# Kernel tuning notes

Measured on AMD Instinct MI355X. Metric: run time of the kernel, lower is better.

The kernel has to match this reference:

```python
import jax, jax.numpy as jnp
import numpy as np

N = 3072          # n_vertices
D = 512           # embedding_size (hardcoded in module)
ALPHA = 0.2       # LeakyReLU slope
AVG_DEG = 32
NEG_INF = -9e15
N_ITERS = 10
TRIPLET_MARGIN = 400.0


def setup_inputs() -> dict:
    key = jax.random.key(0)
    ks = jax.random.split(key, 14)
    s = 0.05  # weight init scale
    emb = jax.random.normal(ks[0], (N, D), dtype=jnp.float32) * 0.1
    # symmetric 0/1 adjacency, no self loops, density ~ AVG_DEG/N
    u = jax.random.uniform(ks[1], (N, N))
    A = jnp.triu((u < (AVG_DEG / N)).astype(jnp.float32), 1)
    adj = A + A.T
    rn = lambda k, shp: jax.random.normal(k, shp, dtype=jnp.float32) * s
    return {
        "embeddings": emb,
        "adj": adj,
        "W_n": rn(ks[2], (D, D)), "a_src_n": rn(ks[3], (D,)), "a_dst_n": rn(ks[4], (D,)),
        "W_nn": rn(ks[5], (D, D)), "a_src_nn": rn(ks[6], (D,)), "a_dst_nn": rn(ks[7], (D,)),
        "W_u": rn(ks[8], (2 * D, D)), "b_u": jnp.zeros((D,), dtype=jnp.float32),
        "W_g": rn(ks[9], (D, D)), "a_src_g": rn(ks[10], (D,)), "a_dst_g": rn(ks[11], (D,)),
    }


def _gat_attention(h, adj, W, a_src, a_dst):
    # standard pyGAT layer: Wh = hW; e_ij = LeakyReLU(a_src.Wh_i + a_dst.Wh_j)
    Wh = h @ W                                   # [N, D]
    e = jax.nn.leaky_relu((Wh @ a_src)[:, None] + (Wh @ a_dst)[None, :], ALPHA)
    att = jax.nn.softmax(jnp.where(adj > 0, e, NEG_INF), axis=1)  # [N, N]
    return att, Wh


def reference(embeddings, adj, W_n, a_src_n, a_dst_n, W_nn, a_src_nn, a_dst_nn,
              W_u, b_u, W_g, a_src_g, a_dst_g):
    n = embeddings.shape[0]
    inv_adj = 1.0 - adj - jnp.eye(n, dtype=adj.dtype)  # non-neighbors, no self
    emb = embeddings
    for _ in range(N_ITERS):
        att_n, Wh_n = _gat_attention(emb, adj, W_n, a_src_n, a_dst_n)
        neigh = jax.nn.elu(att_n @ Wh_n)               # concat=True -> ELU
        att_nn, Wh_nn = _gat_attention(emb, inv_adj, W_nn, a_src_nn, a_dst_nn)
        non_neigh = jax.nn.elu(att_nn @ Wh_nn)
        cat = jnp.concatenate([neigh, non_neigh], axis=1)  # [N, 2D]
        emb = jax.nn.relu(emb + cat @ W_u + b_u)
    sq = jnp.sum(emb * emb, axis=1)
    d2 = sq[:, None] + sq[None, :] - 2.0 * (emb @ emb.T)
    dist = jnp.sqrt(jnp.maximum(d2, 1e-12))            # [N, N]
    embedding_loss = jnp.sum(dist * (-adj))
    triplet_loss = jnp.maximum(embedding_loss + TRIPLET_MARGIN, 0.0)
    # glimpse layer returns the attention matrix itself
    att_g, _ = _gat_attention(emb, adj, W_g, a_src_g, a_dst_g)
    confidence = jnp.max(att_g, axis=1)
    log_conf = jnp.mean(jnp.log(confidence + 1e-8) - jnp.log(1e-8))
    return jnp.stack([triplet_loss, embedding_loss, log_conf])
```

## Files before the change

kernel.cpp:

```cpp
#include <hip/hip_runtime.h>
#include <math.h>

#define N_V 3072
#define D_E 512
#define EDGE_CAP 128
constexpr float LRELU_ALPHA = 0.2f;
constexpr float NEG_INF_F = -9e15f;

typedef __attribute__((ext_vector_type(8))) short bf16x8;
typedef __attribute__((ext_vector_type(4))) float f32x4;
typedef __attribute__((ext_vector_type(4))) unsigned short ushort4v;
typedef __attribute__((ext_vector_type(2))) unsigned short ushort2v;

__device__ inline unsigned short f2bf(float f) {
    union { float f; unsigned int u; } x; x.f = f;
    unsigned int r = x.u + 0x7fffu + ((x.u >> 16) & 1u);
    return (unsigned short)(r >> 16);
}
__device__ inline float bf2f(unsigned short b) {
    union { unsigned int u; float f; } x; x.u = ((unsigned int)b) << 16;
    return x.f;
}

__device__ inline void xcd_swizzle(int& bx, int& by) {
    int gx = gridDim.x, nwg = gx * gridDim.y;
    int flat = by * gx + bx;
    int q = nwg >> 3;
    int swz = (flat & 7) * q + (flat >> 3);
    bx = swz % gx; by = swz / gx;
}

template<int EPI>
__global__ __launch_bounds__(256) void gemm_bf16(
    const unsigned short* __restrict__ A,
    const unsigned short* __restrict__ BT,
    int M, int N, int K,
    unsigned short* __restrict__ C0, int ldc0,
    unsigned short* __restrict__ C1,
    const float* __restrict__ addv,
    const float* __restrict__ bias,
    float* __restrict__ Cf)
{
    constexpr int BM = 128, BN = 64, BK = 64;
    __shared__ unsigned short As[BM * BK];
    __shared__ unsigned short Bs[BN * BK];
    const int tid  = threadIdx.x;
    int bxi = blockIdx.x, byi = blockIdx.y;
    xcd_swizzle(bxi, byi);
    const int bm   = byi * BM, bn = bxi * BN;
    const int lane = tid & 63, wid = tid >> 6;
    const int wr   = wid >> 1, wc = wid & 1;
    const int lr   = lane & 15, lk = lane >> 4;

    f32x4 acc[4][2];
    #pragma unroll
    for (int i = 0; i < 4; ++i)
        #pragma unroll
        for (int j = 0; j < 2; ++j)
            acc[i][j] = (f32x4)(0.f);

    auto asp = (__attribute__((address_space(3))) unsigned short*)As;
    auto bsp = (__attribute__((address_space(3))) unsigned short*)Bs;

    for (int k0 = 0; k0 < K; k0 += BK) {
        #pragma unroll
        for (int l = 0; l < 4; ++l) {
            int li = l * 256 + tid;
            int row = li >> 3, slot = li & 7;
            int gs = slot ^ (row & 7);
            __builtin_amdgcn_global_load_lds(
                (const __attribute__((address_space(1))) void*)(A + (size_t)(bm + row) * K + k0 + gs * 8),
                (__attribute__((address_space(3))) void*)(asp + li * 8), 16, 0, 0);
        }
        #pragma unroll
        for (int l = 0; l < 2; ++l) {
            int li = l * 256 + tid;
            int row = li >> 3, slot = li & 7;
            int gs = slot ^ (row & 7);
            __builtin_amdgcn_global_load_lds(
                (const __attribute__((address_space(1))) void*)(BT + (size_t)(bn + row) * K + k0 + gs * 8),
                (__attribute__((address_space(3))) void*)(bsp + li * 8), 16, 0, 0);
        }
        __syncthreads();

        #pragma unroll
        for (int ks = 0; ks < 2; ++ks) {
            bf16x8 af[4], bfr[2];
            #pragma unroll
            for (int fm = 0; fm < 4; ++fm) {
                int row = wr * 64 + fm * 16 + lr;
                int sl = (ks * 4 + lk) ^ (row & 7);
                af[fm] = *(const bf16x8*)(As + row * BK + sl * 8);
            }
            #pragma unroll
            for (int fn = 0; fn < 2; ++fn) {
                int col = wc * 32 + fn * 16 + lr;
                int sl = (ks * 4 + lk) ^ (col & 7);
                bfr[fn] = *(const bf16x8*)(Bs + col * BK + sl * 8);
            }
            #pragma unroll
            for (int fm = 0; fm < 4; ++fm)
                #pragma unroll
                for (int fn = 0; fn < 2; ++fn)
                    acc[fm][fn] = __builtin_amdgcn_mfma_f32_16x16x32_bf16(
                        af[fm], bfr[fn], acc[fm][fn], 0, 0, 0);
        }
        __syncthreads();
    }

    #pragma unroll
    for (int fm = 0; fm < 4; ++fm) {
        #pragma unroll
        for (int fn = 0; fn < 2; ++fn) {
            int row0 = bm + wr * 64 + fm * 16 + lk * 4;
            int col  = bn + wc * 32 + fn * 16 + lr;
            f32x4 v = acc[fm][fn];
            if (EPI == 2) {
                #pragma unroll
                for (int r = 0; r < 4; ++r) {
                    float x = v[r] + addv[(size_t)(row0 + r) * N + col] + bias[col];
                    x = x > 0.f ? x : 0.f;
                    Cf[(size_t)(row0 + r) * N + col] = x;
                    C0[(size_t)(row0 + r) * ldc0 + col] = f2bf(x);
                }
            } else {
                if (col < 512) {
                    #pragma unroll
                    for (int r = 0; r < 4; ++r)
                        C0[(size_t)(row0 + r) * ldc0 + col] = f2bf(v[r]);
                } else {
                    ushort4v p;
                    p.x = f2bf(v[0]); p.y = f2bf(v[1]);
                    p.z = f2bf(v[2]); p.w = f2bf(v[3]);
                    *(ushort4v*)(C1 + (size_t)(col - 512) * M + row0) = p;
                }
            }
        }
    }
}

__global__ __launch_bounds__(256) void gemm_bf16_sk(
    const unsigned short* __restrict__ A,
    const unsigned short* __restrict__ BT,
    int M, int N, int K,
    float* __restrict__ Cp)
{
    constexpr int BM = 128, BN = 64, BK = 64;
    __shared__ unsigned short As[BM * BK];
    __shared__ unsigned short Bs[BN * BK];
    const int tid  = threadIdx.x;
    int bxi = blockIdx.x, byi = blockIdx.y;
    xcd_swizzle(bxi, byi);
    const int bm   = byi * BM, bn = bxi * BN;
    const int kz   = blockIdx.z;
    const int kh   = K >> 1;
    const int kbeg = kz * kh, kend = kbeg + kh;
    const int lane = tid & 63, wid = tid >> 6;
    const int wr   = wid >> 1, wc = wid & 1;
    const int lr   = lane & 15, lk = lane >> 4;

    f32x4 acc[4][2];
    #pragma unroll
    for (int i = 0; i < 4; ++i)
        #pragma unroll
        for (int j = 0; j < 2; ++j)
            acc[i][j] = (f32x4)(0.f);

    auto asp = (__attribute__((address_space(3))) unsigned short*)As;
    auto bsp = (__attribute__((address_space(3))) unsigned short*)Bs;

    for (int k0 = kbeg; k0 < kend; k0 += BK) {
        #pragma unroll
        for (int l = 0; l < 4; ++l) {
            int li = l * 256 + tid;
            int row = li >> 3, slot = li & 7;
            int gs = slot ^ (row & 7);
            __builtin_amdgcn_global_load_lds(
                (const __attribute__((address_space(1))) void*)(A + (size_t)(bm + row) * K + k0 + gs * 8),
                (__attribute__((address_space(3))) void*)(asp + li * 8), 16, 0, 0);
        }
        #pragma unroll
        for (int l = 0; l < 2; ++l) {
            int li = l * 256 + tid;
            int row = li >> 3, slot = li & 7;
            int gs = slot ^ (row & 7);
            __builtin_amdgcn_global_load_lds(
                (const __attribute__((address_space(1))) void*)(BT + (size_t)(bn + row) * K + k0 + gs * 8),
                (__attribute__((address_space(3))) void*)(bsp + li * 8), 16, 0, 0);
        }
        __syncthreads();

        #pragma unroll
        for (int ks = 0; ks < 2; ++ks) {
            bf16x8 af[4], bfr[2];
            #pragma unroll
            for (int fm = 0; fm < 4; ++fm) {
                int row = wr * 64 + fm * 16 + lr;
                int sl = (ks * 4 + lk) ^ (row & 7);
                af[fm] = *(const bf16x8*)(As + row * BK + sl * 8);
            }
            #pragma unroll
            for (int fn = 0; fn < 2; ++fn) {
                int col = wc * 32 + fn * 16 + lr;
                int sl = (ks * 4 + lk) ^ (col & 7);
                bfr[fn] = *(const bf16x8*)(Bs + col * BK + sl * 8);
            }
            #pragma unroll
            for (int fm = 0; fm < 4; ++fm)
                #pragma unroll
                for (int fn = 0; fn < 2; ++fn)
                    acc[fm][fn] = __builtin_amdgcn_mfma_f32_16x16x32_bf16(
                        af[fm], bfr[fn], acc[fm][fn], 0, 0, 0);
        }
        __syncthreads();
    }

    float* Cz = Cp + (size_t)kz * M * N;
    #pragma unroll
    for (int fm = 0; fm < 4; ++fm) {
        #pragma unroll
        for (int fn = 0; fn < 2; ++fn) {
            int row0 = bm + wr * 64 + fm * 16 + lk * 4;
            int col  = bn + wc * 32 + fn * 16 + lr;
            #pragma unroll
            for (int r = 0; r < 4; ++r)
                Cz[(size_t)(row0 + r) * N + col] = acc[fm][fn][r];
        }
    }
}

__global__ __launch_bounds__(256) void elu_combine(
    const float* __restrict__ p0, const float* __restrict__ p1,
    unsigned short* __restrict__ cat)
{
    int idx = blockIdx.x * 256 + threadIdx.x;
    float4 a = ((const float4*)p0)[idx];
    float4 b = ((const float4*)p1)[idx];
    int r = idx >> 7;
    int c = (idx & 127) * 4;
    float v[4] = { a.x + b.x, a.y + b.y, a.z + b.z, a.w + b.w };
    ushort4v o;
    #pragma unroll
    for (int q = 0; q < 4; ++q) {
        float x = v[q];
        x = x > 0.f ? x : (expf(x) - 1.f);
        ((unsigned short*)&o)[q] = f2bf(x);
    }
    *(ushort4v*)(cat + (size_t)r * (2 * D_E) + D_E + c) = o;
}

__global__ __launch_bounds__(256) void convT_f32_bf16(
    const float* __restrict__ W, unsigned short* __restrict__ WT, int K, int Nw)
{
    int k = blockIdx.x * 256 + threadIdx.x;
    int n = blockIdx.y;
    if (k < K) WT[(size_t)n * K + k] = f2bf(W[(size_t)k * Nw + n]);
}

__global__ __launch_bounds__(256) void conv_bf16(
    const float* __restrict__ X, unsigned short* __restrict__ Y, int n)
{
    int i = blockIdx.x * 256 + threadIdx.x;
    if (i < n) Y[i] = f2bf(X[i]);
}

__global__ __launch_bounds__(256) void build_graph(
    const float* __restrict__ adj, int* __restrict__ edges,
    int* __restrict__ deg, unsigned int* __restrict__ bitmask)
{
    const int i = blockIdx.x, t = threadIdx.x;
    __shared__ int cnts[256];
    unsigned int word = 0;
    int c = 0;
    if (t < 96) {
        #pragma unroll
        for (int b = 0; b < 32; ++b) {
            int j = t * 32 + b;
            if (adj[(size_t)i * N_V + j] > 0.f) { word |= (1u << b); ++c; }
        }
    }
    cnts[t] = c;
    __syncthreads();
    for (int o = 1; o < 256; o <<= 1) {
        int add = (t >= o) ? cnts[t - o] : 0;
        __syncthreads();
        cnts[t] += add;
        __syncthreads();
    }
    int base = cnts[t] - c;
    if (t < 96) {
        int k = 0;
        #pragma unroll
        for (int b = 0; b < 32; ++b) {
            if ((word >> b) & 1u) {
                int pos = base + k;
                if (pos < EDGE_CAP) edges[(size_t)i * EDGE_CAP + pos] = t * 32 + b;
                ++k;
            }
        }
        bitmask[(size_t)i * 96 + t] = word;
    }
    if (t == 0) deg[i] = cnts[255] < EDGE_CAP ? cnts[255] : EDGE_CAP;
}

__global__ __launch_bounds__(256) void matvec6(
    const float* __restrict__ W_n, const float* __restrict__ W_nn,
    const float* __restrict__ W_g,
    const float* __restrict__ as_n, const float* __restrict__ ad_n,
    const float* __restrict__ as_nn, const float* __restrict__ ad_nn,
    const float* __restrict__ as_g, const float* __restrict__ ad_g,
    float* __restrict__ wv)
{
    const int wave = threadIdx.x >> 6, lane = threadIdx.x & 63;
    const int r = blockIdx.x * 4 + wave;
    float a0 = 0, a1 = 0, a2 = 0, a3 = 0, a4 = 0, a5 = 0;
    #pragma unroll
    for (int k = 0; k < 8; ++k) {
        int c = lane + k * 64;
        float wn = W_n[(size_t)r * D_E + c];
        float wm = W_nn[(size_t)r * D_E + c];
        float wg = W_g[(size_t)r * D_E + c];
        a0 = fmaf(wn, as_n[c], a0);  a1 = fmaf(wn, ad_n[c], a1);
        a2 = fmaf(wm, as_nn[c], a2); a3 = fmaf(wm, ad_nn[c], a3);
        a4 = fmaf(wg, as_g[c], a4);  a5 = fmaf(wg, ad_g[c], a5);
    }
    #pragma unroll
    for (int off = 32; off; off >>= 1) {
        a0 += __shfl_down(a0, off); a1 += __shfl_down(a1, off);
        a2 += __shfl_down(a2, off); a3 += __shfl_down(a3, off);
        a4 += __shfl_down(a4, off); a5 += __shfl_down(a5, off);
    }
    if (lane == 0) {
        wv[0 * D_E + r] = a0; wv[1 * D_E + r] = a1;
        wv[2 * D_E + r] = a2; wv[3 * D_E + r] = a3;
        wv[4 * D_E + r] = a4; wv[5 * D_E + r] = a5;
    }
}

template<int NV>
__global__ __launch_bounds__(256) void sd_dots(
    const unsigned short* __restrict__ emb, const float* __restrict__ wv,
    float* __restrict__ outs)
{
    const int wave = threadIdx.x >> 6, lane = threadIdx.x & 63;
    const int i = blockIdx.x * 4 + wave;
    float acc[NV];
    #pragma unroll
    for (int v = 0; v < NV; ++v) acc[v] = 0.f;
    #pragma unroll
    for (int k = 0; k < 8; ++k) {
        int c = lane + k * 64;
        float x = bf2f(emb[(size_t)i * D_E + c]);
        #pragma unroll
        for (int v = 0; v < NV; ++v) acc[v] = fmaf(x, wv[v * D_E + c], acc[v]);
    }
    #pragma unroll
    for (int off = 32; off; off >>= 1)
        #pragma unroll
        for (int v = 0; v < NV; ++v) acc[v] += __shfl_down(acc[v], off);
    if (lane == 0)
        #pragma unroll
        for (int v = 0; v < NV; ++v) outs[v * N_V + i] = acc[v];
}

__global__ __launch_bounds__(256) void nn_sm_gather(
    const unsigned int* __restrict__ bitmask,
    const int* __restrict__ edges, const int* __restrict__ deg,
    const float* __restrict__ sd,
    const unsigned short* __restrict__ Whn,
    unsigned short* __restrict__ att, unsigned short* __restrict__ cat)
{
    const int t = threadIdx.x;
    __shared__ float red[256];
    if (blockIdx.x < N_V) {
        const int i = blockIdx.x;
        const float* s = sd + 2 * N_V;
        const float* dvec = sd + 3 * N_V;
        __shared__ unsigned int mrow[96];
        if (t < 96) mrow[t] = bitmask[(size_t)i * 96 + t];
        __syncthreads();
        const float si = s[i];
        const float4* dv4 = (const float4*)dvec;
        float e[3][4];
        float mloc = -3.4e38f;
        #pragma unroll
        for (int l = 0; l < 3; ++l) {
            int jv = t + l * 256;
            float4 d = dv4[jv];
            int j0 = jv * 4;
            unsigned int w = mrow[j0 >> 5];
            #pragma unroll
            for (int c = 0; c < 4; ++c) {
                int j = j0 + c;
                bool keep = (((w >> (j & 31)) & 1u) == 0u) && (j != i);
                float x = si + ((const float*)&d)[c];
                x = x > 0.f ? x : LRELU_ALPHA * x;
                e[l][c] = keep ? x : NEG_INF_F;
                mloc = fmaxf(mloc, e[l][c]);
            }
        }
        red[t] = mloc; __syncthreads();
        for (int o = 128; o; o >>= 1) {
            if (t < o) red[t] = fmaxf(red[t], red[t + o]);
            __syncthreads();
        }
        float m = red[0]; __syncthreads();
        float zloc = 0.f;
        #pragma unroll
        for (int l = 0; l < 3; ++l)
            #pragma unroll
            for (int c = 0; c < 4; ++c) { e[l][c] = expf(e[l][c] - m); zloc += e[l][c]; }
        red[t] = zloc; __syncthreads();
        for (int o = 128; o; o >>= 1) {
            if (t < o) red[t] += red[t + o];
            __syncthreads();
        }
        const float zinv = 1.f / red[0];
        #pragma unroll
        for (int l = 0; l < 3; ++l) {
            int jv = t + l * 256;
            ushort4v p;
            p.x = f2bf(e[l][0] * zinv); p.y = f2bf(e[l][1] * zinv);
            p.z = f2bf(e[l][2] * zinv); p.w = f2bf(e[l][3] * zinv);
            *(ushort4v*)(att + (size_t)i * N_V + (size_t)jv * 4) = p;
        }
    } else {
        const int i = blockIdx.x - N_V;
        const float* s = sd;
        const float* dvec = sd + N_V;
        const int cnt = deg[i];
        __shared__ float p[EDGE_CAP];
        __shared__ int lst[EDGE_CAP];
        float ev = -3.4e38f;
        if (t < cnt) {
            int j = edges[(size_t)i * EDGE_CAP + t];
            lst[t] = j;
            float x = s[i] + dvec[j];
            x = x > 0.f ? x : LRELU_ALPHA * x;
            p[t] = x;
            ev = x;
        }
        red[t] = ev; __syncthreads();
        for (int o = 128; o; o >>= 1) {
            if (t < o) red[t] = fmaxf(red[t], red[t + o]);
            __syncthreads();
        }
        float m = red[0]; __syncthreads();
        float pe = 0.f;
        if (t < cnt) { pe = expf(p[t] - m); p[t] = pe; }
        red[t] = pe; __syncthreads();
        for (int o = 128; o; o >>= 1) {
            if (t < o) red[t] += red[t + o];
            __syncthreads();
        }
        const float zinv = 1.f / red[0];
        float a0 = 0.f, a1 = 0.f;
        for (int e = 0; e < cnt; ++e) {
            int j = lst[e];
            float w = p[e] * zinv;
            ushort2v h = *(const ushort2v*)(Whn + (size_t)j * D_E + t * 2);
            a0 = fmaf(w, bf2f(h.x), a0);
            a1 = fmaf(w, bf2f(h.y), a1);
        }
        a0 = a0 > 0.f ? a0 : (expf(a0) - 1.f);
        a1 = a1 > 0.f ? a1 : (expf(a1) - 1.f);
        ushort2v o2; o2.x = f2bf(a0); o2.y = f2bf(a1);
        *(ushort2v*)(cat + (size_t)i * (2 * D_E) + t * 2) = o2;
    }
}

__global__ __launch_bounds__(256) void rowsumsq(
    const float* __restrict__ emb, float* __restrict__ sq)
{
    const int wave = threadIdx.x >> 6, lane = threadIdx.x & 63;
    const int row = blockIdx.x * 4 + wave;
    const float* w = emb + (size_t)row * D_E;
    float ss = 0.f;
    #pragma unroll
    for (int k = 0; k < 8; ++k) {
        float x = w[lane + k * 64];
        ss = fmaf(x, x, ss);
    }
    #pragma unroll
    for (int off = 32; off; off >>= 1) ss += __shfl_down(ss, off);
    if (lane == 0) sq[row] = ss;
}

__global__ __launch_bounds__(256) void edge_loss2(
    const int* __restrict__ edges, const int* __restrict__ deg,
    const float* __restrict__ emb, const float* __restrict__ sq,
    float* __restrict__ accum)
{
    __shared__ float wsum[4];
    const int i = blockIdx.x, t = threadIdx.x;
    const int wave = t >> 6, lane = t & 63;
    const int cnt = deg[i];
    float ei[8];
    #pragma unroll
    for (int k = 0; k < 8; ++k) ei[k] = emb[(size_t)i * D_E + lane + k * 64];
    float sum = 0.f;
    for (int e = wave; e < cnt; e += 4) {
        int j = edges[(size_t)i * EDGE_CAP + e];
        float dot = 0.f;
        #pragma unroll
        for (int k = 0; k < 8; ++k)
            dot = fmaf(ei[k], emb[(size_t)j * D_E + lane + k * 64], dot);
        #pragma unroll
        for (int off = 32; off; off >>= 1) dot += __shfl_down(dot, off);
        if (lane == 0) {
            float d2 = sq[i] + sq[j] - 2.f * dot;
            sum += sqrtf(fmaxf(d2, 1e-12f));
        }
    }
    if (lane == 0) wsum[wave] = sum;
    __syncthreads();
    if (t == 0) atomicAdd(accum, -(wsum[0] + wsum[1] + wsum[2] + wsum[3]));
}

__global__ __launch_bounds__(256) void conf_kernel(
    const unsigned int* __restrict__ bitmask, const float* __restrict__ s,
    const float* __restrict__ dvec, float* __restrict__ accum)
{
    const int i = blockIdx.x, t = threadIdx.x;
    __shared__ unsigned int mrow[96];
    __shared__ float red[256];
    if (t < 96) mrow[t] = bitmask[(size_t)i * 96 + t];
    __syncthreads();
    const float si = s[i];
    const float4* dv4 = (const float4*)dvec;
    float e[3][4];
    float mloc = -3.4e38f;
    #pragma unroll
    for (int l = 0; l < 3; ++l) {
        int jv = t + l * 256;
        float4 d = dv4[jv];
        int j0 = jv * 4;
        unsigned int w = mrow[j0 >> 5];
        #pragma unroll
        for (int c = 0; c < 4; ++c) {
            int j = j0 + c;
            bool keep = ((w >> (j & 31)) & 1u) != 0u;
            float x = si + ((const float*)&d)[c];
            x = x > 0.f ? x : LRELU_ALPHA * x;
            e[l][c] = keep ? x : NEG_INF_F;
            mloc = fmaxf(mloc, e[l][c]);
        }
    }
    red[t] = mloc; __syncthreads();
    for (int o = 128; o; o >>= 1) {
        if (t < o) red[t] = fmaxf(red[t], red[t + o]);
        __syncthreads();
    }
    float m = red[0]; __syncthreads();
    float zloc = 0.f;
    #pragma unroll
    for (int l = 0; l < 3; ++l)
        #pragma unroll
        for (int c = 0; c < 4; ++c) zloc += expf(e[l][c] - m);
    red[t] = zloc; __syncthreads();
    for (int o = 128; o; o >>= 1) {
        if (t < o) red[t] += red[t + o];
        __syncthreads();
    }
    if (t == 0) atomicAdd(accum, logf(1.f / red[0] + 1e-8f));
}

__global__ void finalize(const float* __restrict__ accum, float* __restrict__ out)
{
    float loss = accum[0];
    out[0] = fmaxf(loss + 400.f, 0.f);
    out[1] = loss;
    out[2] = accum[1] / (float)N_V - logf(1e-8f);
}

extern "C" void kernel_launch(void* const* d_in, const int* in_sizes, int n_in,
                              void* d_out, int out_size, void* d_ws, size_t ws_size,
                              hipStream_t stream) {
    const float* emb_in   = (const float*)d_in[0];
    const float* adj      = (const float*)d_in[1];
    const float* W_n      = (const float*)d_in[2];
    const float* a_src_n  = (const float*)d_in[3];
    const float* a_dst_n  = (const float*)d_in[4];
    const float* W_nn     = (const float*)d_in[5];
    const float* a_src_nn = (const float*)d_in[6];
    const float* a_dst_nn = (const float*)d_in[7];
    const float* W_u      = (const float*)d_in[8];
    const float* b_u      = (const float*)d_in[9];
    const float* W_g      = (const float*)d_in[10];
    const float* a_src_g  = (const float*)d_in[11];
    const float* a_dst_g  = (const float*)d_in[12];
    float* out = (float*)d_out;

    char* p = (char*)d_ws;
    auto alloc = [&](size_t bytes) { char* r = p; p += (bytes + 255) & ~(size_t)255; return r; };

    unsigned short* att_nn  = (unsigned short*)alloc((size_t)N_V * N_V * 2);
    float*          Cp      = (float*)alloc((size_t)2 * N_V * D_E * 4);
    unsigned short* Whn     = (unsigned short*)alloc((size_t)N_V * D_E * 2);
    unsigned short* WhTnn   = (unsigned short*)alloc((size_t)D_E * N_V * 2);
    unsigned short* cat_bf  = (unsigned short*)alloc((size_t)N_V * 2 * D_E * 2);
    float*          embf[2] = { (float*)alloc((size_t)N_V * D_E * 4),
                                (float*)alloc((size_t)N_V * D_E * 4) };
    unsigned short* embb[2] = { (unsigned short*)alloc((size_t)N_V * D_E * 2),
                                (unsigned short*)alloc((size_t)N_V * D_E * 2) };
    unsigned short* W2T     = (unsigned short*)alloc((size_t)(2 * D_E) * D_E * 2);
    unsigned short* WuT     = (unsigned short*)alloc((size_t)D_E * (2 * D_E) * 2);
    float*          wv      = (float*)alloc(6 * D_E * 4);
    float*          sd      = (float*)alloc(4 * N_V * 4);
    float*          sdg     = (float*)alloc(2 * N_V * 4);
    float*          sq      = (float*)alloc(N_V * 4);
    int*            edges   = (int*)alloc((size_t)N_V * EDGE_CAP * 4);
    int*            deg     = (int*)alloc(N_V * 4);
    unsigned int*   bitmask = (unsigned int*)alloc((size_t)N_V * 96 * 4);
    float*          accum   = (float*)alloc(2 * 4);

    dim3 blk(256);

    convT_f32_bf16<<<dim3(2, D_E), blk, 0, stream>>>(W_n, W2T, D_E, D_E);
    convT_f32_bf16<<<dim3(2, D_E), blk, 0, stream>>>(W_nn, W2T + (size_t)D_E * D_E, D_E, D_E);
    convT_f32_bf16<<<dim3(4, D_E), blk, 0, stream>>>(W_u, WuT, 2 * D_E, D_E);
    conv_bf16<<<(N_V * D_E) / 256, blk, 0, stream>>>(emb_in, embb[0], N_V * D_E);
    hipMemcpyAsync(embf[0], emb_in, (size_t)N_V * D_E * 4, hipMemcpyDeviceToDevice, stream);
    hipMemsetAsync(accum, 0, 2 * sizeof(float), stream);
    build_graph<<<N_V, blk, 0, stream>>>(adj, edges, deg, bitmask);
    matvec6<<<D_E / 4, blk, 0, stream>>>(W_n, W_nn, W_g, a_src_n, a_dst_n,
                                         a_src_nn, a_dst_nn, a_src_g, a_dst_g, wv);

    dim3 gW2(16, N_V / 128);
    dim3 gG(8, N_V / 128);
    dim3 gSK(8, N_V / 128, 2);

    int cur = 0;
    for (int it = 0; it < 10; ++it) {
        int nxt = cur ^ 1;
        sd_dots<4><<<N_V / 4, blk, 0, stream>>>(embb[cur], wv, sd);
        gemm_bf16<4><<<gW2, blk, 0, stream>>>(embb[cur], W2T, N_V, 2 * D_E, D_E,
                                              Whn, D_E, WhTnn, nullptr, nullptr, nullptr);
        nn_sm_gather<<<2 * N_V, blk, 0, stream>>>(bitmask, edges, deg, sd,
                                                  Whn, att_nn, cat_bf);
        gemm_bf16_sk<<<gSK, blk, 0, stream>>>(att_nn, WhTnn, N_V, D_E, N_V, Cp);
        elu_combine<<<(N_V * D_E) / (4 * 256), blk, 0, stream>>>(
            Cp, Cp + (size_t)N_V * D_E, cat_bf);
        gemm_bf16<2><<<gG, blk, 0, stream>>>(cat_bf, WuT, N_V, D_E, 2 * D_E,
                                             embb[nxt], D_E, nullptr, embf[cur], b_u, embf[nxt]);
        cur = nxt;
    }

    rowsumsq<<<N_V / 4, blk, 0, stream>>>(embf[cur], sq);
    edge_loss2<<<N_V, blk, 0, stream>>>(edges, deg, embf[cur], sq, accum);
    sd_dots<2><<<N_V / 4, blk, 0, stream>>>(embb[cur], wv + 4 * D_E, sdg);
    conf_kernel<<<N_V, blk, 0, stream>>>(bitmask, sdg, sdg + N_V, accum + 1);

    finalize<<<1, 1, 0, stream>>>(accum, out);
}
```

Measured before the change: 942.9 us.

## Generate non-neighbor attention on the fly inside GEMM via factored softmax

The non-neighbor attention matrix is no longer written to a dense N×N bf16 buffer. The LeakyReLU softmax is factored into per-row scalars (R1, R0, computed from a global max and the row sums minus the neighbor corrections) and per-column exponentials (ed1, ed0). The GEMM then builds A-tiles in registers from the adjacency bitmask. This removes a large write and read of the attention matrix each iteration, and the GEMM moves to 128x128 tiles with split-K of 4. In exchange it adds top2/zrow kernels, redundant per-element exp-free recomputation in the GEMM, bitmask loads from global inside the inner loop, and possible numerical differences from the global-max factorisation. The edge loss kernel is also reworked to use 16-lane groups with shared memory.

```diff
diff --git a/kernel.cpp b/kernel.cpp
--- a/kernel.cpp
+++ b/kernel.cpp
@@ -139,48 +139,52 @@
     }
 }
 
-__global__ __launch_bounds__(256) void gemm_bf16_sk(
-    const unsigned short* __restrict__ A,
+template<int SPLITK>
+__global__ __launch_bounds__(256) void gemm_nn(
     const unsigned short* __restrict__ BT,
-    int M, int N, int K,
+    const float* __restrict__ dvec,
+    const float* __restrict__ ed1v, const float* __restrict__ ed0v,
+    const float* __restrict__ svec,
+    const float* __restrict__ R1v, const float* __restrict__ R0v,
+    const unsigned int* __restrict__ bitmask,
     float* __restrict__ Cp)
 {
-    constexpr int BM = 128, BN = 64, BK = 64;
-    __shared__ unsigned short As[BM * BK];
+    constexpr int BM = 128, BN = 128, BK = 64;
     __shared__ unsigned short Bs[BN * BK];
-    const int tid  = threadIdx.x;
+    __shared__ float dsh[BK], e1sh[BK], e0sh[BK];
+    const int tid = threadIdx.x;
     int bxi = blockIdx.x, byi = blockIdx.y;
     xcd_swizzle(bxi, byi);
-    const int bm   = byi * BM, bn = bxi * BN;
-    const int kz   = blockIdx.z;
-    const int kh   = K >> 1;
-    const int kbeg = kz * kh, kend = kbeg + kh;
+    const int bm = byi * BM, bn = bxi * BN;
+    const int K  = N_V;
+    const int kh = K / SPLITK;
+    const int kbeg = blockIdx.z * kh, kend = kbeg + kh;
     const int lane = tid & 63, wid = tid >> 6;
-    const int wr   = wid >> 1, wc = wid & 1;
-    const int lr   = lane & 15, lk = lane >> 4;
-
-    f32x4 acc[4][2];
+    const int wr = wid >> 1, wc = wid & 1;
+    const int lr = lane & 15, lk = lane >> 4;
+
+    int   rows[4];
+    float sR[4], r1R[4], r0R[4];
+    #pragma unroll
+    for (int fm = 0; fm < 4; ++fm) {
+        rows[fm] = bm + wr * 64 + fm * 16 + lr;
+        sR[fm]  = svec[rows[fm]];
+        r1R[fm] = R1v[rows[fm]];
+        r0R[fm] = R0v[rows[fm]];
+    }
+
+    f32x4 acc[4][4];
     #pragma unroll
     for (int i = 0; i < 4; ++i)
         #pragma unroll
-        for (int j = 0; j < 2; ++j)
+        for (int j = 0; j < 4; ++j)
             acc[i][j] = (f32x4)(0.f);
 
-    auto asp = (__attribute__((address_space(3))) unsigned short*)As;
     auto bsp = (__attribute__((address_space(3))) unsigned short*)Bs;
 
     for (int k0 = kbeg; k0 < kend; k0 += BK) {
         #pragma unroll
         for (int l = 0; l < 4; ++l) {
-            int li = l * 256 + tid;
-            int row = li >> 3, slot = li & 7;
-            int gs = slot ^ (row & 7);
-            __builtin_amdgcn_global_load_lds(
-                (const __attribute__((address_space(1))) void*)(A + (size_t)(bm + row) * K + k0 + gs * 8),
-                (__attribute__((address_space(3))) void*)(asp + li * 8), 16, 0, 0);
-        }
-        #pragma unroll
-        for (int l = 0; l < 2; ++l) {
             int li = l * 256 + tid;
             int row = li >> 3, slot = li & 7;
             int gs = slot ^ (row & 7);
@@ -188,57 +192,76 @@
                 (const __attribute__((address_space(1))) void*)(BT + (size_t)(bn + row) * K + k0 + gs * 8),
                 (__attribute__((address_space(3))) void*)(bsp + li * 8), 16, 0, 0);
         }
+        if (tid < 64)        dsh[tid]        = dvec[k0 + tid];
+        else if (tid < 128)  e1sh[tid - 64]  = ed1v[k0 + tid - 64];
+        else if (tid < 192)  e0sh[tid - 128] = ed0v[k0 + tid - 128];
         __syncthreads();
 
         #pragma unroll
         for (int ks = 0; ks < 2; ++ks) {
-            bf16x8 af[4], bfr[2];
+            const int kbl = ks * 32 + lk * 8;
+            const int kg  = k0 + kbl;
+            bf16x8 af[4];
             #pragma unroll
             for (int fm = 0; fm < 4; ++fm) {
-                int row = wr * 64 + fm * 16 + lr;
-                int sl = (ks * 4 + lk) ^ (row & 7);
-                af[fm] = *(const bf16x8*)(As + row * BK + sl * 8);
+                unsigned int word = bitmask[(size_t)rows[fm] * 96 + (kg >> 5)];
+                int rel = rows[fm] - (kg & ~31);
+                if ((unsigned)rel < 32u) word |= (1u << rel);
+                unsigned int bits = word >> (lk * 8);
+                #pragma unroll
+                for (int e = 0; e < 8; ++e) {
+                    float dk = dsh[kbl + e];
+                    bool pos = (sR[fm] + dk) > 0.f;
+                    float v = pos ? r1R[fm] * e1sh[kbl + e]
+                                  : r0R[fm] * e0sh[kbl + e];
+                    if ((bits >> e) & 1u) v = 0.f;
+                    af[fm][e] = (short)f2bf(v);
+                }
             }
+            bf16x8 bfr[4];
             #pragma unroll
-            for (int fn = 0; fn < 2; ++fn) {
-                int col = wc * 32 + fn * 16 + lr;
+            for (int fn = 0; fn < 4; ++fn) {
+                int col = wc * 64 + fn * 16 + lr;
                 int sl = (ks * 4 + lk) ^ (col & 7);
                 bfr[fn] = *(const bf16x8*)(Bs + col * BK + sl * 8);
             }
             #pragma unroll
             for (int fm = 0; fm < 4; ++fm)
                 #pragma unroll
-                for (int fn = 0; fn < 2; ++fn)
+                for (int fn = 0; fn < 4; ++fn)
                     acc[fm][fn] = __builtin_amdgcn_mfma_f32_16x16x32_bf16(
                         af[fm], bfr[fn], acc[fm][fn], 0, 0, 0);
         }
         __syncthreads();
     }
 
-    float* Cz = Cp + (size_t)kz * M * N;
+    float* Cz = Cp + (size_t)blockIdx.z * N_V * D_E;
     #pragma unroll
     for (int fm = 0; fm < 4; ++fm) {
         #pragma unroll
-        for (int fn = 0; fn < 2; ++fn) {
+        for (int fn = 0; fn < 4; ++fn) {
             int row0 = bm + wr * 64 + fm * 16 + lk * 4;
-            int col  = bn + wc * 32 + fn * 16 + lr;
+            int col  = bn + wc * 64 + fn * 16 + lr;
             #pragma unroll
             for (int r = 0; r < 4; ++r)
-                Cz[(size_t)(row0 + r) * N + col] = acc[fm][fn][r];
-        }
-    }
-}
-
-__global__ __launch_bounds__(256) void elu_combine(
-    const float* __restrict__ p0, const float* __restrict__ p1,
-    unsigned short* __restrict__ cat)
+                Cz[(size_t)(row0 + r) * D_E + col] = acc[fm][fn][r];
+        }
+    }
+}
+
+__global__ __launch_bounds__(256) void elu_combine4(
+    const float* __restrict__ Cp, unsigned short* __restrict__ cat)
 {
     int idx = blockIdx.x * 256 + threadIdx.x;
-    float4 a = ((const float4*)p0)[idx];
-    float4 b = ((const float4*)p1)[idx];
+    const size_t S = (size_t)N_V * D_E;
+    float4 a = ((const float4*)Cp)[idx];
+    float4 b = ((const float4*)(Cp + S))[idx];
+    float4 c = ((const float4*)(Cp + 2 * S))[idx];
+    float4 d = ((const float4*)(Cp + 3 * S))[idx];
     int r = idx >> 7;
-    int c = (idx & 127) * 4;
-    float v[4] = { a.x + b.x, a.y + b.y, a.z + b.z, a.w + b.w };
+    int cc = (idx & 127) * 4;
+    float v[4] = { a.x + b.x + c.x + d.x, a.y + b.y + c.y + d.y,
+                   a.z + b.z + c.z + d.z, a.w + b.w + c.w + d.w };
     ushort4v o;
     #pragma unroll
     for (int q = 0; q < 4; ++q) {
@@ -246,7 +269,101 @@
         x = x > 0.f ? x : (expf(x) - 1.f);
         ((unsigned short*)&o)[q] = f2bf(x);
     }
-    *(ushort4v*)(cat + (size_t)r * (2 * D_E) + D_E + c) = o;
+    *(ushort4v*)(cat + (size_t)r * (2 * D_E) + D_E + cc) = o;
+}
+
+__global__ __launch_bounds__(256) void top2_ed(
+    const float* __restrict__ d, float* __restrict__ topbuf,
+    float* __restrict__ ed1, float* __restrict__ ed0)
+{
+    const int t = threadIdx.x;
+    float m1 = -3.4e38f, m2 = -3.4e38f; int a1 = -1;
+    for (int it = 0; it < 12; ++it) {
+        int j = t + it * 256;
+        float v = d[j];
+        if (v > m1) { m2 = m1; m1 = v; a1 = j; }
+        else if (v > m2) m2 = v;
+    }
+    __shared__ float m1s[256], m2s[256];
+    __shared__ int a1s[256];
+    m1s[t] = m1; m2s[t] = m2; a1s[t] = a1;
+    __syncthreads();
+    for (int o = 128; o; o >>= 1) {
+        if (t < o) {
+            float bm1 = m1s[t + o], bm2 = m2s[t + o]; int ba1 = a1s[t + o];
+            if (bm1 > m1s[t]) {
+                m2s[t] = fmaxf(m1s[t], bm2);
+                m1s[t] = bm1; a1s[t] = ba1;
+            } else {
+                m2s[t] = fmaxf(m2s[t], bm1);
+            }
+        }
+        __syncthreads();
+    }
+    float dmax = m1s[0];
+    if (t == 0) {
+        topbuf[0] = dmax; topbuf[1] = m2s[0];
+        topbuf[2] = __int_as_float(a1s[0]);
+    }
+    for (int it = 0; it < 12; ++it) {
+        int j = t + it * 256;
+        float x = d[j] - dmax;
+        ed1[j] = expf(x);
+        ed0[j] = expf(0.2f * x);
+    }
+}
+
+__global__ __launch_bounds__(256) void nn_zrow(
+    const float* __restrict__ d, const float* __restrict__ ed1,
+    const float* __restrict__ ed0, const float* __restrict__ s,
+    const int* __restrict__ edges, const int* __restrict__ deg,
+    const float* __restrict__ topbuf,
+    float* __restrict__ R1, float* __restrict__ R0)
+{
+    const int wave = threadIdx.x >> 6, lane = threadIdx.x & 63;
+    const int i = blockIdx.x * 4 + wave;
+    const float si = s[i];
+    float S1 = 0.f, S0 = 0.f;
+    #pragma unroll
+    for (int it = 0; it < 48; ++it) {
+        int j = lane + it * 64;
+        float dj = d[j];
+        bool pos = (si + dj) > 0.f;
+        S1 += pos ? ed1[j] : 0.f;
+        S0 += pos ? 0.f : ed0[j];
+    }
+    float C1 = 0.f, C0 = 0.f;
+    const int cnt = deg[i];
+    for (int e = lane; e < cnt; e += 64) {
+        int j = edges[(size_t)i * EDGE_CAP + e];
+        float dj = d[j];
+        bool pos = (si + dj) > 0.f;
+        C1 += pos ? ed1[j] : 0.f;
+        C0 += pos ? 0.f : ed0[j];
+    }
+    if (lane == 63) {
+        float dj = d[i];
+        bool pos = (si + dj) > 0.f;
+        C1 += pos ? ed1[i] : 0.f;
+        C0 += pos ? 0.f : ed0[i];
+    }
+    #pragma unroll
+    for (int off = 32; off; off >>= 1) {
+        S1 += __shfl_down(S1, off); S0 += __shfl_down(S0, off);
+        C1 += __shfl_down(C1, off); C0 += __shfl_down(C0, off);
+    }
+    if (lane == 0) {
+        float dmax = topbuf[0], d2max = topbuf[1];
+        int amax = __float_as_int(topbuf[2]);
+        float dmx = (i == amax) ? d2max : dmax;
+        float x = si + dmx;
+        float m = x > 0.f ? x : LRELU_ALPHA * x;
+        float r1 = expf(si + dmax - m);
+        float r0 = expf(LRELU_ALPHA * (si + dmax) - m);
+        float Z = r1 * (S1 - C1) + r0 * (S0 - C0);
+        Z = fmaxf(Z, 1e-35f);
+        R1[i] = r1 / Z; R0[i] = r0 / Z;
+    }
 }
 
 __global__ __launch_bounds__(256) void convT_f32_bf16(
@@ -363,110 +480,51 @@
         for (int v = 0; v < NV; ++v) outs[v * N_V + i] = acc[v];
 }
 
-__global__ __launch_bounds__(256) void nn_sm_gather(
-    const unsigned int* __restrict__ bitmask,
+__global__ __launch_bounds__(256) void neigh_gather(
     const int* __restrict__ edges, const int* __restrict__ deg,
-    const float* __restrict__ sd,
-    const unsigned short* __restrict__ Whn,
-    unsigned short* __restrict__ att, unsigned short* __restrict__ cat)
-{
-    const int t = threadIdx.x;
+    const float* __restrict__ s, const float* __restrict__ dvec,
+    const unsigned short* __restrict__ Whn, unsigned short* __restrict__ cat)
+{
+    const int i = blockIdx.x, t = threadIdx.x;
+    const int cnt = deg[i];
+    __shared__ float p[EDGE_CAP];
+    __shared__ int lst[EDGE_CAP];
     __shared__ float red[256];
-    if (blockIdx.x < N_V) {
-        const int i = blockIdx.x;
-        const float* s = sd + 2 * N_V;
-        const float* dvec = sd + 3 * N_V;
-        __shared__ unsigned int mrow[96];
-        if (t < 96) mrow[t] = bitmask[(size_t)i * 96 + t];
-        __syncthreads();
-        const float si = s[i];
-        const float4* dv4 = (const float4*)dvec;
-        float e[3][4];
-        float mloc = -3.4e38f;
-        #pragma unroll
-        for (int l = 0; l < 3; ++l) {
-            int jv = t + l * 256;
-            float4 d = dv4[jv];
-            int j0 = jv * 4;
-            unsigned int w = mrow[j0 >> 5];
-            #pragma unroll
-            for (int c = 0; c < 4; ++c) {
-                int j = j0 + c;
-                bool keep = (((w >> (j & 31)) & 1u) == 0u) && (j != i);
-                float x = si + ((const float*)&d)[c];
-                x = x > 0.f ? x : LRELU_ALPHA * x;
-                e[l][c] = keep ? x : NEG_INF_F;
-                mloc = fmaxf(mloc, e[l][c]);
-            }
-        }
-        red[t] = mloc; __syncthreads();
-        for (int o = 128; o; o >>= 1) {
-            if (t < o) red[t] = fmaxf(red[t], red[t + o]);
-            __syncthreads();
-        }
-        float m = red[0]; __syncthreads();
-        float zloc = 0.f;
-        #pragma unroll
-        for (int l = 0; l < 3; ++l)
-            #pragma unroll
-            for (int c = 0; c < 4; ++c) { e[l][c] = expf(e[l][c] - m); zloc += e[l][c]; }
-        red[t] = zloc; __syncthreads();
-        for (int o = 128; o; o >>= 1) {
-            if (t < o) red[t] += red[t + o];
-            __syncthreads();
-        }
-        const float zinv = 1.f / red[0];
-        #pragma unroll
-        for (int l = 0; l < 3; ++l) {
-            int jv = t + l * 256;
-            ushort4v p;
-            p.x = f2bf(e[l][0] * zinv); p.y = f2bf(e[l][1] * zinv);
-            p.z = f2bf(e[l][2] * zinv); p.w = f2bf(e[l][3] * zinv);
-            *(ushort4v*)(att + (size_t)i * N_V + (size_t)jv * 4) = p;
-        }
-    } else {
-        const int i = blockIdx.x - N_V;
-        const float* s = sd;
-        const float* dvec = sd + N_V;
-        const int cnt = deg[i];
-        __shared__ float p[EDGE_CAP];
-        __shared__ int lst[EDGE_CAP];
-        float ev = -3.4e38f;
-        if (t < cnt) {
-            int j = edges[(size_t)i * EDGE_CAP + t];
-            lst[t] = j;
-            float x = s[i] + dvec[j];
-            x = x > 0.f ? x : LRELU_ALPHA * x;
-            p[t] = x;
-            ev = x;
-        }
-        red[t] = ev; __syncthreads();
-        for (int o = 128; o; o >>= 1) {
-            if (t < o) red[t] = fmaxf(red[t], red[t + o]);
-            __syncthreads();
-        }
-        float m = red[0]; __syncthreads();
-        float pe = 0.f;
-        if (t < cnt) { pe = expf(p[t] - m); p[t] = pe; }
-        red[t] = pe; __syncthreads();
-        for (int o = 128; o; o >>= 1) {
-            if (t < o) red[t] += red[t + o];
-            __syncthreads();
-        }
-        const float zinv = 1.f / red[0];
-        float a0 = 0.f, a1 = 0.f;
-        for (int e = 0; e < cnt; ++e) {
-            int j = lst[e];
-            float w = p[e] * zinv;
-            ushort2v h = *(const ushort2v*)(Whn + (size_t)j * D_E + t * 2);
-            a0 = fmaf(w, bf2f(h.x), a0);
-            a1 = fmaf(w, bf2f(h.y), a1);
-        }
-        a0 = a0 > 0.f ? a0 : (expf(a0) - 1.f);
-        a1 = a1 > 0.f ? a1 : (expf(a1) - 1.f);
-        ushort2v o2; o2.x = f2bf(a0); o2.y = f2bf(a1);
-        *(ushort2v*)(cat + (size_t)i * (2 * D_E) + t * 2) = o2;
-    }
+    float ev = -3.4e38f;
+    if (t < cnt) {
+        int j = edges[(size_t)i * EDGE_CAP + t];
+        lst[t] = j;
+        float x = s[i] + dvec[j];
+        x = x > 0.f ? x : LRELU_ALPHA * x;
+        p[t] = x;
+        ev = x;
+    }
+    red[t] = ev; __syncthreads();
+    for (int o = 128; o; o >>= 1) {
+        if (t < o) red[t] = fmaxf(red[t], red[t + o]);
+        __syncthreads();
+    }
+    float m = red[0]; __syncthreads();
+    float pe = 0.f;
+    if (t < cnt) { pe = expf(p[t] - m); p[t] = pe; }
+    red[t] = pe; __syncthreads();
+    for (int o = 128; o; o >>= 1) {
+        if (t < o) red[t] += red[t + o];
+        __syncthreads();
+    }
+    const float zinv = 1.f / red[0];
+    float a0 = 0.f, a1 = 0.f;
+    for (int e = 0; e < cnt; ++e) {
+        int j = lst[e];
+        float w = p[e] * zinv;
+        ushort2v h = *(const ushort2v*)(Whn + (size_t)j * D_E + t * 2);
+        a0 = fmaf(w, bf2f(h.x), a0);
+        a1 = fmaf(w, bf2f(h.y), a1);
+    }
+    a0 = a0 > 0.f ? a0 : (expf(a0) - 1.f);
+    a1 = a1 > 0.f ? a1 : (expf(a1) - 1.f);
+    ushort2v o2; o2.x = f2bf(a0); o2.y = f2bf(a1);
+    *(ushort2v*)(cat + (size_t)i * (2 * D_E) + t * 2) = o2;
 }
 
 __global__ __launch_bounds__(256) void rowsumsq(
@@ -486,35 +544,44 @@
     if (lane == 0) sq[row] = ss;
 }
 
-__global__ __launch_bounds__(256) void edge_loss2(
+__global__ __launch_bounds__(256) void edge_loss3(
     const int* __restrict__ edges, const int* __restrict__ deg,
     const float* __restrict__ emb, const float* __restrict__ sq,
     float* __restrict__ accum)
 {
-    __shared__ float wsum[4];
+    __shared__ float eish[D_E];
+    __shared__ float gsum[16];
     const int i = blockIdx.x, t = threadIdx.x;
-    const int wave = t >> 6, lane = t & 63;
+    if (t < 128) ((float4*)eish)[t] = ((const float4*)(emb + (size_t)i * D_E))[t];
+    __syncthreads();
+    const int g = t >> 4, l = t & 15;
     const int cnt = deg[i];
-    float ei[8];
-    #pragma unroll
-    for (int k = 0; k < 8; ++k) ei[k] = emb[(size_t)i * D_E + lane + k * 64];
     float sum = 0.f;
-    for (int e = wave; e < cnt; e += 4) {
+    for (int e = g; e < cnt; e += 16) {
         int j = edges[(size_t)i * EDGE_CAP + e];
         float dot = 0.f;
         #pragma unroll
-        for (int k = 0; k < 8; ++k)
-            dot = fmaf(ei[k], emb[(size_t)j * D_E + lane + k * 64], dot);
-        #pragma unroll
-        for (int off = 32; off; off >>= 1) dot += __shfl_down(dot, off);
-        if (lane == 0) {
+        for (int q = 0; q < 8; ++q) {
+            int off = q * 64 + l * 4;
+            float4 a = *(const float4*)(eish + off);
+            float4 b = *(const float4*)(emb + (size_t)j * D_E + off);
+            dot += a.x * b.x + a.y * b.y + a.z * b.z + a.w * b.w;
+        }
+        #pragma unroll
+        for (int msk = 1; msk < 16; msk <<= 1) dot += __shfl_xor(dot, msk);
+        if (l == 0) {
             float d2 = sq[i] + sq[j] - 2.f * dot;
             sum += sqrtf(fmaxf(d2, 1e-12f));
         }
     }
-    if (lane == 0) wsum[wave] = sum;
+    if (l == 0) gsum[g] = sum;
     __syncthreads();
-    if (t == 0) atomicAdd(accum, -(wsum[0] + wsum[1] + wsum[2] + wsum[3]));
+    if (t == 0) {
+        float tot = 0.f;
+        #pragma unroll
+        for (int k = 0; k < 16; ++k) tot += gsum[k];
+        atomicAdd(accum, -tot);
+    }
 }
 
 __global__ __launch_bounds__(256) void conf_kernel(
@@ -594,8 +661,7 @@
     char* p = (char*)d_ws;
     auto alloc = [&](size_t bytes) { char* r = p; p += (bytes + 255) & ~(size_t)255; return r; };
 
-    unsigned short* att_nn  = (unsigned short*)alloc((size_t)N_V * N_V * 2);
-    float*          Cp      = (float*)alloc((size_t)2 * N_V * D_E * 4);
+    float*          Cp      = (float*)alloc((size_t)4 * N_V * D_E * 4);
     unsigned short* Whn     = (unsigned short*)alloc((size_t)N_V * D_E * 2);
     unsigned short* WhTnn   = (unsigned short*)alloc((size_t)D_E * N_V * 2);
     unsigned short* cat_bf  = (unsigned short*)alloc((size_t)N_V * 2 * D_E * 2);
@@ -609,6 +675,11 @@
     float*          sd      = (float*)alloc(4 * N_V * 4);
     float*          sdg     = (float*)alloc(2 * N_V * 4);
     float*          sq      = (float*)alloc(N_V * 4);
+    float*          ed1     = (float*)alloc(N_V * 4);
+    float*          ed0     = (float*)alloc(N_V * 4);
+    float*          R1      = (float*)alloc(N_V * 4);
+    float*          R0      = (float*)alloc(N_V * 4);
+    float*          topbuf  = (float*)alloc(4 * 4);
     int*            edges   = (int*)alloc((size_t)N_V * EDGE_CAP * 4);
     int*            deg     = (int*)alloc(N_V * 4);
     unsigned int*   bitmask = (unsigned int*)alloc((size_t)N_V * 96 * 4);
@@ -628,7 +699,10 @@
 
     dim3 gW2(16, N_V / 128);
     dim3 gG(8, N_V / 128);
-    dim3 gSK(8, N_V / 128, 2);
+    dim3 gNN(4, N_V / 128, 4);
+
+    const float* d_nn = sd + 3 * N_V;
+    const float* s_nn = sd + 2 * N_V;
 
     int cur = 0;
     for (int it = 0; it < 10; ++it) {
@@ -636,18 +710,20 @@
         sd_dots<4><<<N_V / 4, blk, 0, stream>>>(embb[cur], wv, sd);
         gemm_bf16<4><<<gW2, blk, 0, stream>>>(embb[cur], W2T, N_V, 2 * D_E, D_E,
                                               Whn, D_E, WhTnn, nullptr, nullptr, nullptr);
-        nn_sm_gather<<<2 * N_V, blk, 0, stream>>>(bitmask, edges, deg, sd,
-                                                  Whn, att_nn, cat_bf);
-        gemm_bf16_sk<<<gSK, blk, 0, stream>>>(att_nn, WhTnn, N_V, D_E, N_V, Cp);
-        elu_combine<<<(N_V * D_E) / (4 * 256), blk, 0, stream>>>(
-            Cp, Cp + (size_t)N_V * D_E, cat_bf);
+        top2_ed<<<1, blk, 0, stream>>>(d_nn, topbuf, ed1, ed0);
+        nn_zrow<<<N_V / 4, blk, 0, stream>>>(d_nn, ed1, ed0, s_nn,
+                                             edges, deg, topbuf, R1, R0);
+        neigh_gather<<<N_V, blk, 0, stream>>>(edges, deg, sd, sd + N_V, Whn, cat_bf);
+        gemm_nn<4><<<gNN, blk, 0, stream>>>(WhTnn, d_nn, ed1, ed0, s_nn,
+                                            R1, R0, bitmask, Cp);
+        elu_combine4<<<(N_V * D_E) / (4 * 256), blk, 0, stream>>>(Cp, cat_bf);
         gemm_bf16<2><<<gG, blk, 0, stream>>>(cat_bf, WuT, N_V, D_E, 2 * D_E,
                                              embb[nxt], D_E, nullptr, embf[cur], b_u, embf[nxt]);
         cur = nxt;
     }
 
     rowsumsq<<<N_V / 4, blk, 0, stream>>>(embf[cur], sq);
-    edge_loss2<<<N_V, blk, 0, stream>>>(edges, deg, embf[cur], sq, accum);
+    edge_loss3<<<N_V, blk, 0, stream>>>(edges, deg, embf[cur], sq, accum);
     sd_dots<2><<<N_V / 4, blk, 0, stream>>>(embb[cur], wv + 4 * D_E, sdg);
     conf_kernel<<<N_V, blk, 0, stream>>>(bitmask, sdg, sdg + N_V, accum + 1);
 
```

New measurement: 1.682 ms. 1.78x slower.

## Widen split-K GEMM tile to 128x128 with 4-way split; rework edge loss via centered bf16

Applied to the files above, without the earlier changes.

The non-neighbor attention GEMM now uses 128x128 tiles with a four-way K split instead of 128x64 tiles with two-way, so each block does more MFMA work per LDS load. The combine kernel now sums four partial buffers. The final edge loss no longer uses row norms; it centers the embeddings by the column mean, stores them as bf16 and computes squared differences directly with 16 lanes per edge. The wider tile raises register pressure and the extra partials double the fp32 scratch traffic, while the bf16 distance path trades precision for bandwidth.

```diff
diff --git a/kernel.cpp b/kernel.cpp
--- a/kernel.cpp
+++ b/kernel.cpp
@@ -139,31 +139,31 @@
     }
 }
 
+template<int SPLITK>
 __global__ __launch_bounds__(256) void gemm_bf16_sk(
     const unsigned short* __restrict__ A,
     const unsigned short* __restrict__ BT,
     int M, int N, int K,
     float* __restrict__ Cp)
 {
-    constexpr int BM = 128, BN = 64, BK = 64;
+    constexpr int BM = 128, BN = 128, BK = 64;
     __shared__ unsigned short As[BM * BK];
     __shared__ unsigned short Bs[BN * BK];
     const int tid  = threadIdx.x;
     int bxi = blockIdx.x, byi = blockIdx.y;
     xcd_swizzle(bxi, byi);
     const int bm   = byi * BM, bn = bxi * BN;
-    const int kz   = blockIdx.z;
-    const int kh   = K >> 1;
-    const int kbeg = kz * kh, kend = kbeg + kh;
+    const int kh   = K / SPLITK;
+    const int kbeg = blockIdx.z * kh, kend = kbeg + kh;
     const int lane = tid & 63, wid = tid >> 6;
     const int wr   = wid >> 1, wc = wid & 1;
     const int lr   = lane & 15, lk = lane >> 4;
 
-    f32x4 acc[4][2];
+    f32x4 acc[4][4];
     #pragma unroll
     for (int i = 0; i < 4; ++i)
         #pragma unroll
-        for (int j = 0; j < 2; ++j)
+        for (int j = 0; j < 4; ++j)
             acc[i][j] = (f32x4)(0.f);
 
     auto asp = (__attribute__((address_space(3))) unsigned short*)As;
@@ -180,7 +180,7 @@
                 (__attribute__((address_space(3))) void*)(asp + li * 8), 16, 0, 0);
         }
         #pragma unroll
-        for (int l = 0; l < 2; ++l) {
+        for (int l = 0; l < 4; ++l) {
             int li = l * 256 + tid;
             int row = li >> 3, slot = li & 7;
             int gs = slot ^ (row & 7);
@@ -192,7 +192,7 @@
 
         #pragma unroll
         for (int ks = 0; ks < 2; ++ks) {
-            bf16x8 af[4], bfr[2];
+            bf16x8 af[4], bfr[4];
             #pragma unroll
             for (int fm = 0; fm < 4; ++fm) {
                 int row = wr * 64 + fm * 16 + lr;
@@ -200,28 +200,28 @@
                 af[fm] = *(const bf16x8*)(As + row * BK + sl * 8);
             }
             #pragma unroll
-            for (int fn = 0; fn < 2; ++fn) {
-                int col = wc * 32 + fn * 16 + lr;
+            for (int fn = 0; fn < 4; ++fn) {
+                int col = wc * 64 + fn * 16 + lr;
                 int sl = (ks * 4 + lk) ^ (col & 7);
                 bfr[fn] = *(const bf16x8*)(Bs + col * BK + sl * 8);
             }
             #pragma unroll
             for (int fm = 0; fm < 4; ++fm)
                 #pragma unroll
-                for (int fn = 0; fn < 2; ++fn)
+                for (int fn = 0; fn < 4; ++fn)
                     acc[fm][fn] = __builtin_amdgcn_mfma_f32_16x16x32_bf16(
                         af[fm], bfr[fn], acc[fm][fn], 0, 0, 0);
         }
         __syncthreads();
     }
 
-    float* Cz = Cp + (size_t)kz * M * N;
+    float* Cz = Cp + (size_t)blockIdx.z * M * N;
     #pragma unroll
     for (int fm = 0; fm < 4; ++fm) {
         #pragma unroll
-        for (int fn = 0; fn < 2; ++fn) {
+        for (int fn = 0; fn < 4; ++fn) {
             int row0 = bm + wr * 64 + fm * 16 + lk * 4;
-            int col  = bn + wc * 32 + fn * 16 + lr;
+            int col  = bn + wc * 64 + fn * 16 + lr;
             #pragma unroll
             for (int r = 0; r < 4; ++r)
                 Cz[(size_t)(row0 + r) * N + col] = acc[fm][fn][r];
@@ -229,16 +229,19 @@
     }
 }
 
-__global__ __launch_bounds__(256) void elu_combine(
-    const float* __restrict__ p0, const float* __restrict__ p1,
-    unsigned short* __restrict__ cat)
+__global__ __launch_bounds__(256) void elu_combine4(
+    const float* __restrict__ Cp, unsigned short* __restrict__ cat)
 {
     int idx = blockIdx.x * 256 + threadIdx.x;
-    float4 a = ((const float4*)p0)[idx];
-    float4 b = ((const float4*)p1)[idx];
+    const size_t S = (size_t)N_V * D_E;
+    float4 a = ((const float4*)Cp)[idx];
+    float4 b = ((const float4*)(Cp + S))[idx];
+    float4 c = ((const float4*)(Cp + 2 * S))[idx];
+    float4 d = ((const float4*)(Cp + 3 * S))[idx];
     int r = idx >> 7;
-    int c = (idx & 127) * 4;
-    float v[4] = { a.x + b.x, a.y + b.y, a.z + b.z, a.w + b.w };
+    int cc = (idx & 127) * 4;
+    float v[4] = { a.x + b.x + c.x + d.x, a.y + b.y + c.y + d.y,
+                   a.z + b.z + c.z + d.z, a.w + b.w + c.w + d.w };
     ushort4v o;
     #pragma unroll
     for (int q = 0; q < 4; ++q) {
@@ -246,7 +249,7 @@
         x = x > 0.f ? x : (expf(x) - 1.f);
         ((unsigned short*)&o)[q] = f2bf(x);
     }
-    *(ushort4v*)(cat + (size_t)r * (2 * D_E) + D_E + c) = o;
+    *(ushort4v*)(cat + (size_t)r * (2 * D_E) + D_E + cc) = o;
 }
 
 __global__ __launch_bounds__(256) void convT_f32_bf16(
@@ -469,52 +472,68 @@
     }
 }
 
-__global__ __launch_bounds__(256) void rowsumsq(
-    const float* __restrict__ emb, float* __restrict__ sq)
-{
-    const int wave = threadIdx.x >> 6, lane = threadIdx.x & 63;
-    const int row = blockIdx.x * 4 + wave;
-    const float* w = emb + (size_t)row * D_E;
-    float ss = 0.f;
-    #pragma unroll
-    for (int k = 0; k < 8; ++k) {
-        float x = w[lane + k * 64];
-        ss = fmaf(x, x, ss);
-    }
-    #pragma unroll
-    for (int off = 32; off; off >>= 1) ss += __shfl_down(ss, off);
-    if (lane == 0) sq[row] = ss;
-}
-
-__global__ __launch_bounds__(256) void edge_loss2(
+__global__ __launch_bounds__(256) void colsum(
+    const float* __restrict__ emb, float* __restrict__ musum)
+{
+    const int b = blockIdx.x, t = threadIdx.x;
+    float s0 = 0.f, s1 = 0.f;
+    for (int r = 0; r < 64; ++r) {
+        const float* row = emb + (size_t)(b * 64 + r) * D_E;
+        s0 += row[t];
+        s1 += row[t + 256];
+    }
+    atomicAdd(&musum[t], s0);
+    atomicAdd(&musum[t + 256], s1);
+}
+
+__global__ __launch_bounds__(256) void center_bf16(
+    const float* __restrict__ emb, const float* __restrict__ musum,
+    unsigned short* __restrict__ embc)
+{
+    int i = blockIdx.x * 256 + threadIdx.x;
+    int c = i & (D_E - 1);
+    embc[i] = f2bf(emb[i] - musum[c] * (1.f / N_V));
+}
+
+__global__ __launch_bounds__(256) void edge_loss_c(
     const int* __restrict__ edges, const int* __restrict__ deg,
-    const float* __restrict__ emb, const float* __restrict__ sq,
-    float* __restrict__ accum)
-{
-    __shared__ float wsum[4];
+    const unsigned short* __restrict__ embc, float* __restrict__ accum)
+{
+    __shared__ unsigned short rowi[D_E];
+    __shared__ float gsum[16];
     const int i = blockIdx.x, t = threadIdx.x;
-    const int wave = t >> 6, lane = t & 63;
+    if (t < 64) ((bf16x8*)rowi)[t] = ((const bf16x8*)(embc + (size_t)i * D_E))[t];
+    __syncthreads();
+    const int g = t >> 4, l = t & 15;
     const int cnt = deg[i];
-    float ei[8];
-    #pragma unroll
-    for (int k = 0; k < 8; ++k) ei[k] = emb[(size_t)i * D_E + lane + k * 64];
     float sum = 0.f;
-    for (int e = wave; e < cnt; e += 4) {
+    for (int e = g; e < cnt; e += 16) {
         int j = edges[(size_t)i * EDGE_CAP + e];
-        float dot = 0.f;
-        #pragma unroll
-        for (int k = 0; k < 8; ++k)
-            dot = fmaf(ei[k], emb[(size_t)j * D_E + lane + k * 64], dot);
-        #pragma unroll
-        for (int off = 32; off; off >>= 1) dot += __shfl_down(dot, off);
-        if (lane == 0) {
-            float d2 = sq[i] + sq[j] - 2.f * dot;
-            sum += sqrtf(fmaxf(d2, 1e-12f));
-        }
-    }
-    if (lane == 0) wsum[wave] = sum;
+        float d2 = 0.f;
+        #pragma unroll
+        for (int q = 0; q < 4; ++q) {
+            int off = q * 128 + l * 8;
+            bf16x8 a = *(const bf16x8*)(rowi + off);
+            bf16x8 b = *(const bf16x8*)(embc + (size_t)j * D_E + off);
+            #pragma unroll
+            for (int k = 0; k < 8; ++k) {
+                float df = bf2f(((unsigned short*)&a)[k]) -
+                           bf2f(((unsigned short*)&b)[k]);
+                d2 = fmaf(df, df, d2);
+            }
+        }
+        #pragma unroll
+        for (int msk = 1; msk < 16; msk <<= 1) d2 += __shfl_xor(d2, msk);
+        if (l == 0) sum += sqrtf(fmaxf(d2, 1e-12f));
+    }
+    if (l == 0) gsum[g] = sum;
     __syncthreads();
-    if (t == 0) atomicAdd(accum, -(wsum[0] + wsum[1] + wsum[2] + wsum[3]));
+    if (t == 0) {
+        float tot = 0.f;
+        #pragma unroll
+        for (int k = 0; k < 16; ++k) tot += gsum[k];
+        atomicAdd(accum, -tot);
+    }
 }
 
 __global__ __launch_bounds__(256) void conf_kernel(
@@ -595,7 +614,7 @@
     auto alloc = [&](size_t bytes) { char* r = p; p += (bytes + 255) & ~(size_t)255; return r; };
 
     unsigned short* att_nn  = (unsigned short*)alloc((size_t)N_V * N_V * 2);
-    float*          Cp      = (float*)alloc((size_t)2 * N_V * D_E * 4);
+    float*          Cp      = (float*)alloc((size_t)4 * N_V * D_E * 4);
     unsigned short* Whn     = (unsigned short*)alloc((size_t)N_V * D_E * 2);
     unsigned short* WhTnn   = (unsigned short*)alloc((size_t)D_E * N_V * 2);
     unsigned short* cat_bf  = (unsigned short*)alloc((size_t)N_V * 2 * D_E * 2);
@@ -603,12 +622,13 @@
                                 (float*)alloc((size_t)N_V * D_E * 4) };
     unsigned short* embb[2] = { (unsigned short*)alloc((size_t)N_V * D_E * 2),
                                 (unsigned short*)alloc((size_t)N_V * D_E * 2) };
+    unsigned short* embc    = (unsigned short*)alloc((size_t)N_V * D_E * 2);
     unsigned short* W2T     = (unsigned short*)alloc((size_t)(2 * D_E) * D_E * 2);
     unsigned short* WuT     = (unsigned short*)alloc((size_t)D_E * (2 * D_E) * 2);
     float*          wv      = (float*)alloc(6 * D_E * 4);
     float*          sd      = (float*)alloc(4 * N_V * 4);
     float*          sdg     = (float*)alloc(2 * N_V * 4);
-    float*          sq      = (float*)alloc(N_V * 4);
+    float*          musum   = (float*)alloc(D_E * 4);
     int*            edges   = (int*)alloc((size_t)N_V * EDGE_CAP * 4);
     int*            deg     = (int*)alloc(N_V * 4);
     unsigned int*   bitmask = (unsigned int*)alloc((size_t)N_V * 96 * 4);
@@ -622,13 +642,14 @@
     conv_bf16<<<(N_V * D_E) / 256, blk, 0, stream>>>(emb_in, embb[0], N_V * D_E);
     hipMemcpyAsync(embf[0], emb_in, (size_t)N_V * D_E * 4, hipMemcpyDeviceToDevice, stream);
     hipMemsetAsync(accum, 0, 2 * sizeof(float), stream);
+    hipMemsetAsync(musum, 0, D_E * sizeof(float), stream);
     build_graph<<<N_V, blk, 0, stream>>>(adj, edges, deg, bitmask);
     matvec6<<<D_E / 4, blk, 0, stream>>>(W_n, W_nn, W_g, a_src_n, a_dst_n,
                                          a_src_nn, a_dst_nn, a_src_g, a_dst_g, wv);
 
     dim3 gW2(16, N_V / 128);
     dim3 gG(8, N_V / 128);
-    dim3 gSK(8, N_V / 128, 2);
+    dim3 gSK(4, N_V / 128, 4);
 
     int cur = 0;
     for (int it = 0; it < 10; ++it) {
@@ -638,16 +659,16 @@
                                               Whn, D_E, WhTnn, nullptr, nullptr, nullptr);
         nn_sm_gather<<<2 * N_V, blk, 0, stream>>>(bitmask, edges, deg, sd,
                                                   Whn, att_nn, cat_bf);
-        gemm_bf16_sk<<<gSK, blk, 0, stream>>>(att_nn, WhTnn, N_V, D_E, N_V, Cp);
-        elu_combine<<<(N_V * D_E) / (4 * 256), blk, 0, stream>>>(
-            Cp, Cp + (size_t)N_V * D_E, cat_bf);
+        gemm_bf16_sk<4><<<gSK, blk, 0, stream>>>(att_nn, WhTnn, N_V, D_E, N_V, Cp);
+        elu_combine4<<<(N_V * D_E) / (4 * 256), blk, 0, stream>>>(Cp, cat_bf);
         gemm_bf16<2><<<gG, blk, 0, stream>>>(cat_bf, WuT, N_V, D_E, 2 * D_E,
                                              embb[nxt], D_E, nullptr, embf[cur], b_u, embf[nxt]);
         cur = nxt;
     }
 
-    rowsumsq<<<N_V / 4, blk, 0, stream>>>(embf[cur], sq);
-    edge_loss2<<<N_V, blk, 0, stream>>>(edges, deg, embf[cur], sq, accum);
+    colsum<<<N_V / 64, blk, 0, stream>>>(embf[cur], musum);
+    center_bf16<<<(N_V * D_E) / 256, blk, 0, stream>>>(embf[cur], musum, embc);
+    edge_loss_c<<<N_V, blk, 0, stream>>>(edges, deg, embc, accum);
     sd_dots<2><<<N_V / 4, blk, 0, stream>>>(embb[cur], wv + 4 * D_E, sdg);
     conf_kernel<<<N_V, blk, 0, stream>>>(bitmask, sdg, sdg + N_V, accum + 1);
 
```

Result: faster. 912.1 us (-3.3%).
